# Optimization experiments

Measured on AMD Instinct MI355X. Metric: run time of the kernel, lower is better.

The kernel has to match this reference:

```python
import jax, jax.numpy as jnp
import numpy as np

N_NODES = 50000
N_EDGES = 500000
NFEAT = 128
NHID = 128
NOUT = 16


def setup_inputs() -> dict:
    key = jax.random.key(0)
    ks = jax.random.split(key, 8)
    x = jax.random.normal(ks[0], (N_NODES, NFEAT), dtype=jnp.float32)
    edge_src = jax.random.randint(ks[1], (N_EDGES,), 0, N_NODES, dtype=jnp.int32)
    edge_dst = jax.random.randint(ks[2], (N_EDGES,), 0, N_NODES, dtype=jnp.int32)
    edge_weight = jax.random.uniform(ks[3], (N_EDGES,), dtype=jnp.float32)
    # Glorot-ish init for linear weights, zero bias (PyG GCNConv default bias=0)
    def glorot(k, fan_in, fan_out):
        s = jnp.sqrt(6.0 / (fan_in + fan_out))
        return jax.random.uniform(k, (fan_in, fan_out), jnp.float32, -s, s)
    W1 = glorot(ks[4], NFEAT, NHID)
    W2 = glorot(ks[5], NHID, NHID)
    W3 = glorot(ks[6], NHID, NOUT)
    b1 = jnp.zeros((NHID,), jnp.float32)
    b2 = jnp.zeros((NHID,), jnp.float32)
    b3 = jnp.zeros((NOUT,), jnp.float32)
    return {"x": x, "edge_src": edge_src, "edge_dst": edge_dst,
            "edge_weight": edge_weight, "W1": W1, "b1": b1,
            "W2": W2, "b2": b2, "W3": W3, "b3": b3}


def gcn_conv(x, src, dst, ew, W, b):
    """PyG GCNConv: symmetric-normalized aggregation with self-loops (weight 1).

    out_i = sum_{(j->i)} d_i^{-1/2} w_ji d_j^{-1/2} (x_j W) + d_i^{-1} (x_i W) + b
    where d_i = 1 + sum of incoming edge weights.
    """
    n = x.shape[0]
    xw = x @ W                                            # [N, F_out]
    deg = jax.ops.segment_sum(ew, dst, num_segments=n) + 1.0  # self-loop weight 1
    dinv = jnp.where(deg > 0, jax.lax.rsqrt(deg), 0.0)    # d^{-1/2}
    norm = dinv[src] * ew * dinv[dst]                     # [E]
    agg = jax.ops.segment_sum(xw[src] * norm[:, None], dst, num_segments=n)
    self_loop = xw * (dinv * dinv)[:, None]               # d_i^{-1} * x_i W
    return agg + self_loop + b


def reference(x, edge_src, edge_dst, edge_weight, W1, b1, W2, b2, W3, b3):
    # Dropout layers are identity in eval mode.
    h = gcn_conv(x, edge_src, edge_dst, edge_weight, W1, b1)
    h = jax.nn.relu(h)
    h = gcn_conv(h, edge_src, edge_dst, edge_weight, W2, b2)
    h = jax.nn.relu(h)
    h = gcn_conv(h, edge_src, edge_dst, edge_weight, W3, b3)
    return jax.nn.log_softmax(h, axis=1)
```

## Files before the change

kernel.cpp:

```cpp
#include <hip/hip_runtime.h>
#include <math.h>

#define NN 50000
#define NE 500000
#define NF 128
#define NO 16
#define SCAN_B 1024
#define NPART 16

typedef _Float16 f16x8 __attribute__((ext_vector_type(8)));
typedef float f32x4 __attribute__((ext_vector_type(4)));


__global__ void k_count_rank(const int* __restrict__ dst, int* __restrict__ pcnt,
                             int* __restrict__ rank, int E) {
    int part = blockIdx.x & (NPART - 1);
    int e = blockIdx.x * blockDim.x + threadIdx.x;
    if (e < E) {
        int d = dst[e];
        rank[e] = atomicAdd(&pcnt[part * NN + d], 1);
    }
}

__global__ void k_combine(int* __restrict__ pcnt, int* __restrict__ counts, int N) {
    int n = blockIdx.x * blockDim.x + threadIdx.x;
    if (n < N) {
        int run = 0;
#pragma unroll
        for (int p = 0; p < NPART; ++p) {
            int v = pcnt[p * NN + n];
            pcnt[p * NN + n] = run;
            run += v;
        }
        counts[n] = run;
    }
}

__global__ void k_scan1(const int* __restrict__ counts, int* __restrict__ offs,
                        int* __restrict__ bsums, int N) {
    __shared__ int s[SCAN_B];
    int t = threadIdx.x;
    int i = blockIdx.x * SCAN_B + t;
    int c = (i < N) ? counts[i] : 0;
    s[t] = c;
    __syncthreads();
    for (int off = 1; off < SCAN_B; off <<= 1) {
        int x = (t >= off) ? s[t - off] : 0;
        __syncthreads();
        s[t] += x;
        __syncthreads();
    }
    if (i < N) offs[i] = s[t] - c;
    if (t == SCAN_B - 1) bsums[blockIdx.x] = s[t];
}

__global__ void k_scan2(int* __restrict__ bsums, int NB) {
    int t = threadIdx.x;
    int v = (t < NB) ? bsums[t] : 0;
    int orig = v;
#pragma unroll
    for (int off = 1; off < 64; off <<= 1) {
        int u = __shfl_up(v, off, 64);
        if (t >= off) v += u;
    }
    if (t < NB) bsums[t] = v - orig;
}

__global__ void k_scan3(int* __restrict__ offs, const int* __restrict__ bsums,
                        int N, int E) {
    int i = blockIdx.x * blockDim.x + threadIdx.x;
    if (i < N) {
        offs[i] = offs[i] + bsums[i >> 10];
    } else if (i == N) {
        offs[N] = E;
    }
}

__global__ void k_scatter(const int* __restrict__ src, const int* __restrict__ dst,
                          const float* __restrict__ ew, const int* __restrict__ offs,
                          const int* __restrict__ pcnt, const int* __restrict__ rank,
                          int* __restrict__ src_s, float* __restrict__ ew_s, int E) {
    int part = blockIdx.x & (NPART - 1);
    int e = blockIdx.x * blockDim.x + threadIdx.x;
    if (e < E) {
        int d = dst[e];
        int p = offs[d] + pcnt[part * NN + d] + rank[e];
        src_s[p] = src[e];
        ew_s[p]  = ew[e];
    }
}

__global__ void k_dinv_csr(const float* __restrict__ ew_s, const int* __restrict__ offs,
                           float* __restrict__ dinv, int N) {
    int n = blockIdx.x * blockDim.x + threadIdx.x;
    if (n < N) {
        float deg = 1.0f;
        int s = offs[n], e = offs[n + 1];
        for (int j = s; j < e; ++j) deg += ew_s[j];
        dinv[n] = rsqrtf(deg);
    }
}

__global__ void k_prep_w(const float* __restrict__ W1, const float* __restrict__ W2,
                         _Float16* __restrict__ W1T, _Float16* __restrict__ W2T) {
    int idx = blockIdx.x * 256 + threadIdx.x;
    int r = idx >> 7, c = idx & 127;
    W1T[(size_t)c * NF + r] = (_Float16)W1[idx];
    W2T[(size_t)c * NF + r] = (_Float16)W2[idx];
}


__device__ inline f16x8 afrag_load(const float* X, int row, int k0) {
    const float4* p = (const float4*)(X + (size_t)row * NF + k0);
    float4 a = p[0], b = p[1];
    f16x8 r;
    r[0] = (_Float16)a.x; r[1] = (_Float16)a.y; r[2] = (_Float16)a.z; r[3] = (_Float16)a.w;
    r[4] = (_Float16)b.x; r[5] = (_Float16)b.y; r[6] = (_Float16)b.z; r[7] = (_Float16)b.w;
    return r;
}
__device__ inline f16x8 afrag_load(const _Float16* X, int row, int k0) {
    return *(const f16x8*)(X + (size_t)row * NF + k0);
}

template <typename TA>
__global__ __launch_bounds__(256) void k_gemm_mfma(const TA* __restrict__ X,
                                                   const _Float16* __restrict__ WT,
                                                   const float* __restrict__ dinv,
                                                   _Float16* __restrict__ Z, int M) {
    __shared__ _Float16 ls[4][16 * NF];
    const int tid  = threadIdx.x;
    const int w    = tid >> 6;
    const int lane = tid & 63;
    const int n16  = lane & 15;
    const int quad = lane >> 4;
    const int r0   = blockIdx.x * 64 + w * 16;

    int arow = r0 + n16; if (arow > M - 1) arow = M - 1;

    f32x4 acc[8];
#pragma unroll
    for (int c = 0; c < 8; ++c) acc[c] = (f32x4){0.f, 0.f, 0.f, 0.f};

#pragma unroll
    for (int kk = 0; kk < 4; ++kk) {
        int k0 = kk * 32 + quad * 8;
        f16x8 a = afrag_load(X, arow, k0);
#pragma unroll
        for (int c = 0; c < 8; ++c) {
            f16x8 b = *(const f16x8*)(WT + (size_t)(c * 16 + n16) * NF + k0);
            acc[c] = __builtin_amdgcn_mfma_f32_16x16x32_f16(a, b, acc[c], 0, 0, 0);
        }
    }

#pragma unroll
    for (int reg = 0; reg < 4; ++reg) {
        int lrow = quad * 4 + reg;
        int grow = r0 + lrow; if (grow > M - 1) grow = M - 1;
        float di = dinv[grow];
#pragma unroll
        for (int c = 0; c < 8; ++c)
            ls[w][lrow * NF + c * 16 + n16] = (_Float16)(acc[c][reg] * di);
    }
    __syncthreads();
#pragma unroll
    for (int i = 0; i < 4; ++i) {
        int off16 = i * 64 + lane;
        int row = off16 >> 4;
        int grow = r0 + row;
        if (grow < M) {
            f16x8 v = *(const f16x8*)(&ls[w][off16 * 8]);
            *(f16x8*)(Z + (size_t)grow * NF + (off16 & 15) * 8) = v;
        }
    }
}

__global__ __launch_bounds__(256) void k_agg128h(const _Float16* __restrict__ z,
                                                 const float* __restrict__ dinv,
                                                 const int* __restrict__ offs,
                                                 const int* __restrict__ src_s,
                                                 const float* __restrict__ ew_s,
                                                 const float* __restrict__ bias,
                                                 _Float16* __restrict__ hout, int relu) {
    const int tid = threadIdx.x;
    const int ln = tid & 63;
    int n = __builtin_amdgcn_readfirstlane(blockIdx.x * 4 + (tid >> 6));

    union CV { unsigned int u; _Float16 h[2]; };

    float di = dinv[n];
    CV sv; sv.u = *(const unsigned int*)(z + (size_t)n * NF + ln * 2);
    float acc0 = (float)sv.h[0];
    float acc1 = (float)sv.h[1];

    int s = offs[n], e = offs[n + 1];
    int j = s;
    for (; j + 3 < e; j += 4) {
        int s0 = src_s[j], s1 = src_s[j + 1], s2 = src_s[j + 2], s3 = src_s[j + 3];
        float w0 = ew_s[j], w1 = ew_s[j + 1], w2 = ew_s[j + 2], w3 = ew_s[j + 3];
        CV u0, u1, u2, u3;
        u0.u = *(const unsigned int*)(z + (size_t)s0 * NF + ln * 2);
        u1.u = *(const unsigned int*)(z + (size_t)s1 * NF + ln * 2);
        u2.u = *(const unsigned int*)(z + (size_t)s2 * NF + ln * 2);
        u3.u = *(const unsigned int*)(z + (size_t)s3 * NF + ln * 2);
        acc0 = fmaf((float)u0.h[0], w0, acc0); acc1 = fmaf((float)u0.h[1], w0, acc1);
        acc0 = fmaf((float)u1.h[0], w1, acc0); acc1 = fmaf((float)u1.h[1], w1, acc1);
        acc0 = fmaf((float)u2.h[0], w2, acc0); acc1 = fmaf((float)u2.h[1], w2, acc1);
        acc0 = fmaf((float)u3.h[0], w3, acc0); acc1 = fmaf((float)u3.h[1], w3, acc1);
    }
    for (; j < e; ++j) {
        int s0 = src_s[j];
        float w0 = ew_s[j];
        CV u0; u0.u = *(const unsigned int*)(z + (size_t)s0 * NF + ln * 2);
        acc0 = fmaf((float)u0.h[0], w0, acc0);
        acc1 = fmaf((float)u0.h[1], w0, acc1);
    }
    float2 bb = *(const float2*)(bias + ln * 2);
    acc0 = fmaf(di, acc0, bb.x);
    acc1 = fmaf(di, acc1, bb.y);
    if (relu) { acc0 = fmaxf(acc0, 0.0f); acc1 = fmaxf(acc1, 0.0f); }
    CV o; o.h[0] = (_Float16)acc0; o.h[1] = (_Float16)acc1;
    *(unsigned int*)(hout + (size_t)n * NF + ln * 2) = o.u;
}

__global__ __launch_bounds__(256) void k_gemm16(const _Float16* __restrict__ H,
                                                const float* __restrict__ W3,
                                                const float* __restrict__ dinv,
                                                float* __restrict__ Z3, int M) {
    __shared__ float Wl[NF * NO];
    __shared__ float Hs[16 * 132];
    int tid = threadIdx.x;
    for (int i = tid; i < NF * NO; i += 256) Wl[i] = W3[i];
    int n0 = blockIdx.x * 16;
    {
        int row = tid >> 4, h8 = tid & 15;
        int gr = n0 + row; if (gr > M - 1) gr = M - 1;
        f16x8 v = *(const f16x8*)(H + (size_t)gr * NF + h8 * 8);
        float4 f0 = {(float)v[0], (float)v[1], (float)v[2], (float)v[3]};
        float4 f1 = {(float)v[4], (float)v[5], (float)v[6], (float)v[7]};
        *(float4*)(&Hs[row * 132 + h8 * 8])     = f0;
        *(float4*)(&Hs[row * 132 + h8 * 8 + 4]) = f1;
    }
    __syncthreads();
    int ln = tid >> 4, c = tid & 15;
    float acc = 0.0f;
#pragma unroll 8
    for (int k = 0; k < NF; ++k) acc = fmaf(Hs[ln * 132 + k], Wl[k * NO + c], acc);
    int n = n0 + ln;
    if (n < M) Z3[(size_t)n * NO + c] = acc * dinv[n];
}

__global__ __launch_bounds__(256) void k_agg16_ls(const float* __restrict__ z3,
                                                  const float* __restrict__ dinv,
                                                  const int* __restrict__ offs,
                                                  const int* __restrict__ src_s,
                                                  const float* __restrict__ ew_s,
                                                  const float* __restrict__ bias,
                                                  float* __restrict__ out) {
    int tid = threadIdx.x;
    int ln = tid >> 4, c = tid & 15;
    int n = blockIdx.x * 16 + ln;
    float acc = z3[(size_t)n * NO + c];
    int s = offs[n], e = offs[n + 1];
    for (int j = s; j < e; ++j) {
        acc = fmaf(z3[(size_t)src_s[j] * NO + c], ew_s[j], acc);
    }
    acc = fmaf(dinv[n], acc, bias[c]);
    float m = acc;
#pragma unroll
    for (int off = 8; off > 0; off >>= 1) m = fmaxf(m, __shfl_xor(m, off, 16));
    float ex = expf(acc - m);
    float ss = ex;
#pragma unroll
    for (int off = 8; off > 0; off >>= 1) ss += __shfl_xor(ss, off, 16);
    out[(size_t)n * NO + c] = acc - m - logf(ss);
}


extern "C" void kernel_launch(void* const* d_in, const int* in_sizes, int n_in,
                              void* d_out, int out_size, void* d_ws, size_t ws_size,
                              hipStream_t stream) {
    const float* x   = (const float*)d_in[0];
    const int*   esrc= (const int*)  d_in[1];
    const int*   edst= (const int*)  d_in[2];
    const float* ew  = (const float*)d_in[3];
    const float* W1  = (const float*)d_in[4];
    const float* b1  = (const float*)d_in[5];
    const float* W2  = (const float*)d_in[6];
    const float* b2  = (const float*)d_in[7];
    const float* W3  = (const float*)d_in[8];
    const float* b3  = (const float*)d_in[9];
    float* out = (float*)d_out;

    char* p = (char*)d_ws;
    _Float16* z   = (_Float16*)p; p += (size_t)NN * NF * 2;
    _Float16* h   = (_Float16*)p; p += (size_t)NN * NF * 2;
    float* z3     = (float*)p; p += (size_t)NN * NO * 4;
    float* dinv   = (float*)p; p += (size_t)NN * 4;
    float* ew_s   = (float*)p; p += (size_t)NE * 4;
    int*   src_s  = (int*)p;   p += (size_t)NE * 4;
    int*   rank   = (int*)p;   p += (size_t)NE * 4;
    int*   pcnt   = (int*)p;   p += (size_t)NPART * NN * 4;
    int*   counts = (int*)p;   p += (size_t)NN * 4;
    int*   offs   = (int*)p;   p += (size_t)(NN + 1) * 4;
    int*   bsums  = (int*)p;   p += 256;
    _Float16* W1T = (_Float16*)p; p += (size_t)NF * NF * 2;
    _Float16* W2T = (_Float16*)p; p += (size_t)NF * NF * 2;

    const int NB  = (NN + SCAN_B - 1) / SCAN_B;
    const int EBL = (NE + 255) / 256;
    const int NBL = (NN + 255) / 256;

    hipMemsetAsync(pcnt, 0, (size_t)NPART * NN * 4, stream);

    k_count_rank<<<EBL, 256, 0, stream>>>(edst, pcnt, rank, NE);
    k_combine<<<NBL, 256, 0, stream>>>(pcnt, counts, NN);
    k_scan1<<<NB, SCAN_B, 0, stream>>>(counts, offs, bsums, NN);
    k_scan2<<<1, 64, 0, stream>>>(bsums, NB);
    k_scan3<<<(NN + 256) / 256, 256, 0, stream>>>(offs, bsums, NN, NE);
    k_scatter<<<EBL, 256, 0, stream>>>(esrc, edst, ew, offs, pcnt, rank, src_s, ew_s, NE);
    k_dinv_csr<<<NBL, 256, 0, stream>>>(ew_s, offs, dinv, NN);
    k_prep_w<<<64, 256, 0, stream>>>(W1, W2, W1T, W2T);

    k_gemm_mfma<float><<<(NN + 63) / 64, 256, 0, stream>>>(x, W1T, dinv, z, NN);
    k_agg128h<<<NN / 4, 256, 0, stream>>>(z, dinv, offs, src_s, ew_s, b1, h, 1);
    k_gemm_mfma<_Float16><<<(NN + 63) / 64, 256, 0, stream>>>(h, W2T, dinv, z, NN);
    k_agg128h<<<NN / 4, 256, 0, stream>>>(z, dinv, offs, src_s, ew_s, b2, h, 1);
    k_gemm16<<<(NN + 15) / 16, 256, 0, stream>>>(h, W3, dinv, z3, NN);
    k_agg16_ls<<<NN / 16, 256, 0, stream>>>(z3, dinv, offs, src_s, ew_s, b3, out);
}
```

Baseline: 266.7 us.

## Fuse CSR build kernels, pack edge records, and store layer-3 features in fp16

Folds the weight transpose into the count kernel, merges the partition combine into the first scan, and bakes the prefix offsets into the per-partition counters so the scatter needs fewer lookups. Source index and weight are packed into one int2 record per edge. The 128-wide aggregation loads 64 records cooperatively per wave and broadcasts them with shuffles instead of loading each one per lane. The 16-wide layer-3 features are stored as fp16, halving gather traffic at some precision cost. Together these cut launch count and memory traffic in the preprocessing and aggregation stages.

```diff
diff --git a/kernel.cpp b/kernel.cpp
--- a/kernel.cpp
+++ b/kernel.cpp
@@ -7,106 +7,110 @@
 #define NO 16
 #define SCAN_B 1024
 #define NPART 16
+#define EBL 1954
 
 typedef _Float16 f16x8 __attribute__((ext_vector_type(8)));
 typedef float f32x4 __attribute__((ext_vector_type(4)));
 
 
 __global__ void k_count_rank(const int* __restrict__ dst, int* __restrict__ pcnt,
-                             int* __restrict__ rank, int E) {
+                             int* __restrict__ rank, int E,
+                             const float* __restrict__ W1, const float* __restrict__ W2,
+                             _Float16* __restrict__ W1T, _Float16* __restrict__ W2T) {
+    int b = blockIdx.x;
+    if (b < EBL) {
+        int part = b & (NPART - 1);
+        int e = b * 256 + threadIdx.x;
+        if (e < E) {
+            int d = dst[e];
+            rank[e] = atomicAdd(&pcnt[part * NN + d], 1);
+        }
+    } else {
+        int idx = (b - EBL) * 256 + threadIdx.x;
+        int r = idx >> 7, c = idx & 127;
+        W1T[(size_t)c * NF + r] = (_Float16)W1[idx];
+        W2T[(size_t)c * NF + r] = (_Float16)W2[idx];
+    }
+}
+
+__global__ void k_scan1f(int* __restrict__ pcnt, int* __restrict__ offs_p,
+                         int* __restrict__ bsums, int N) {
+    __shared__ int sm[SCAN_B];
+    int t = threadIdx.x;
+    int i = blockIdx.x * SCAN_B + t;
+    int c = 0;
+    if (i < N) {
+        int run = 0;
+#pragma unroll
+        for (int p = 0; p < NPART; ++p) {
+            int v = pcnt[p * NN + i];
+            pcnt[p * NN + i] = run;
+            run += v;
+        }
+        c = run;
+    }
+    sm[t] = c;
+    __syncthreads();
+    for (int off = 1; off < SCAN_B; off <<= 1) {
+        int x = (t >= off) ? sm[t - off] : 0;
+        __syncthreads();
+        sm[t] += x;
+        __syncthreads();
+    }
+    if (i < N) offs_p[i] = sm[t] - c;
+    if (t == SCAN_B - 1) bsums[blockIdx.x] = sm[t];
+}
+
+__global__ void k_scan2(int* __restrict__ bsums, int NB) {
+    int t = threadIdx.x;
+    int v = (t < NB) ? bsums[t] : 0;
+    int orig = v;
+#pragma unroll
+    for (int off = 1; off < 64; off <<= 1) {
+        int u = __shfl_up(v, off, 64);
+        if (t >= off) v += u;
+    }
+    if (t < NB) bsums[t] = v - orig;
+}
+
+__global__ void k_scan3x(const int* __restrict__ offs_p, const int* __restrict__ bsums,
+                         int* __restrict__ pcnt, int* __restrict__ offs_f, int E) {
+    int i = blockIdx.x * blockDim.x + threadIdx.x;
+    if (i < NPART * NN) {
+        int p = i / NN;
+        int n = i - p * NN;
+        int v = offs_p[n] + bsums[n >> 10];
+        pcnt[i] += v;
+        if (p == 0) offs_f[n] = v;
+    } else if (i == NPART * NN) {
+        offs_f[NN] = E;
+    }
+}
+
+__global__ void k_scatter(const int* __restrict__ src, const int* __restrict__ dst,
+                          const float* __restrict__ ew, const int* __restrict__ pcnt,
+                          const int* __restrict__ rank, int2* __restrict__ edge_rec, int E) {
     int part = blockIdx.x & (NPART - 1);
     int e = blockIdx.x * blockDim.x + threadIdx.x;
     if (e < E) {
         int d = dst[e];
-        rank[e] = atomicAdd(&pcnt[part * NN + d], 1);
-    }
-}
-
-__global__ void k_combine(int* __restrict__ pcnt, int* __restrict__ counts, int N) {
-    int n = blockIdx.x * blockDim.x + threadIdx.x;
-    if (n < N) {
-        int run = 0;
-#pragma unroll
-        for (int p = 0; p < NPART; ++p) {
-            int v = pcnt[p * NN + n];
-            pcnt[p * NN + n] = run;
-            run += v;
-        }
-        counts[n] = run;
-    }
-}
-
-__global__ void k_scan1(const int* __restrict__ counts, int* __restrict__ offs,
-                        int* __restrict__ bsums, int N) {
-    __shared__ int s[SCAN_B];
-    int t = threadIdx.x;
-    int i = blockIdx.x * SCAN_B + t;
-    int c = (i < N) ? counts[i] : 0;
-    s[t] = c;
-    __syncthreads();
-    for (int off = 1; off < SCAN_B; off <<= 1) {
-        int x = (t >= off) ? s[t - off] : 0;
-        __syncthreads();
-        s[t] += x;
-        __syncthreads();
-    }
-    if (i < N) offs[i] = s[t] - c;
-    if (t == SCAN_B - 1) bsums[blockIdx.x] = s[t];
-}
-
-__global__ void k_scan2(int* __restrict__ bsums, int NB) {
-    int t = threadIdx.x;
-    int v = (t < NB) ? bsums[t] : 0;
-    int orig = v;
-#pragma unroll
-    for (int off = 1; off < 64; off <<= 1) {
-        int u = __shfl_up(v, off, 64);
-        if (t >= off) v += u;
-    }
-    if (t < NB) bsums[t] = v - orig;
-}
-
-__global__ void k_scan3(int* __restrict__ offs, const int* __restrict__ bsums,
-                        int N, int E) {
-    int i = blockIdx.x * blockDim.x + threadIdx.x;
-    if (i < N) {
-        offs[i] = offs[i] + bsums[i >> 10];
-    } else if (i == N) {
-        offs[N] = E;
-    }
-}
-
-__global__ void k_scatter(const int* __restrict__ src, const int* __restrict__ dst,
-                          const float* __restrict__ ew, const int* __restrict__ offs,
-                          const int* __restrict__ pcnt, const int* __restrict__ rank,
-                          int* __restrict__ src_s, float* __restrict__ ew_s, int E) {
-    int part = blockIdx.x & (NPART - 1);
-    int e = blockIdx.x * blockDim.x + threadIdx.x;
-    if (e < E) {
-        int d = dst[e];
-        int p = offs[d] + pcnt[part * NN + d] + rank[e];
-        src_s[p] = src[e];
-        ew_s[p]  = ew[e];
-    }
-}
-
-__global__ void k_dinv_csr(const float* __restrict__ ew_s, const int* __restrict__ offs,
+        int pos = pcnt[part * NN + d] + rank[e];
+        int2 r;
+        r.x = src[e];
+        r.y = __float_as_int(ew[e]);
+        edge_rec[pos] = r;
+    }
+}
+
+__global__ void k_dinv_csr(const int2* __restrict__ edge_rec, const int* __restrict__ offs,
                            float* __restrict__ dinv, int N) {
     int n = blockIdx.x * blockDim.x + threadIdx.x;
     if (n < N) {
         float deg = 1.0f;
         int s = offs[n], e = offs[n + 1];
-        for (int j = s; j < e; ++j) deg += ew_s[j];
+        for (int j = s; j < e; ++j) deg += __int_as_float(edge_rec[j].y);
         dinv[n] = rsqrtf(deg);
     }
-}
-
-__global__ void k_prep_w(const float* __restrict__ W1, const float* __restrict__ W2,
-                         _Float16* __restrict__ W1T, _Float16* __restrict__ W2T) {
-    int idx = blockIdx.x * 256 + threadIdx.x;
-    int r = idx >> 7, c = idx & 127;
-    W1T[(size_t)c * NF + r] = (_Float16)W1[idx];
-    W2T[(size_t)c * NF + r] = (_Float16)W2[idx];
 }
 
 
@@ -177,8 +181,7 @@
 __global__ __launch_bounds__(256) void k_agg128h(const _Float16* __restrict__ z,
                                                  const float* __restrict__ dinv,
                                                  const int* __restrict__ offs,
-                                                 const int* __restrict__ src_s,
-                                                 const float* __restrict__ ew_s,
+                                                 const int2* __restrict__ edge_rec,
                                                  const float* __restrict__ bias,
                                                  _Float16* __restrict__ hout, int relu) {
     const int tid = threadIdx.x;
@@ -188,44 +191,53 @@
     union CV { unsigned int u; _Float16 h[2]; };
 
     float di = dinv[n];
-    CV sv; sv.u = *(const unsigned int*)(z + (size_t)n * NF + ln * 2);
+    CV sv; sv.u = *(const unsigned int*)(z + ((size_t)n << 7) + ln * 2);
     float acc0 = (float)sv.h[0];
     float acc1 = (float)sv.h[1];
 
     int s = offs[n], e = offs[n + 1];
-    int j = s;
-    for (; j + 3 < e; j += 4) {
-        int s0 = src_s[j], s1 = src_s[j + 1], s2 = src_s[j + 2], s3 = src_s[j + 3];
-        float w0 = ew_s[j], w1 = ew_s[j + 1], w2 = ew_s[j + 2], w3 = ew_s[j + 3];
-        CV u0, u1, u2, u3;
-        u0.u = *(const unsigned int*)(z + (size_t)s0 * NF + ln * 2);
-        u1.u = *(const unsigned int*)(z + (size_t)s1 * NF + ln * 2);
-        u2.u = *(const unsigned int*)(z + (size_t)s2 * NF + ln * 2);
-        u3.u = *(const unsigned int*)(z + (size_t)s3 * NF + ln * 2);
-        acc0 = fmaf((float)u0.h[0], w0, acc0); acc1 = fmaf((float)u0.h[1], w0, acc1);
-        acc0 = fmaf((float)u1.h[0], w1, acc0); acc1 = fmaf((float)u1.h[1], w1, acc1);
-        acc0 = fmaf((float)u2.h[0], w2, acc0); acc1 = fmaf((float)u2.h[1], w2, acc1);
-        acc0 = fmaf((float)u3.h[0], w3, acc0); acc1 = fmaf((float)u3.h[1], w3, acc1);
-    }
-    for (; j < e; ++j) {
-        int s0 = src_s[j];
-        float w0 = ew_s[j];
-        CV u0; u0.u = *(const unsigned int*)(z + (size_t)s0 * NF + ln * 2);
-        acc0 = fmaf((float)u0.h[0], w0, acc0);
-        acc1 = fmaf((float)u0.h[1], w0, acc1);
+    for (int base = s; base < e; base += 64) {
+        int cnt = e - base; if (cnt > 64) cnt = 64;
+        int2 rec = {0, 0};
+        if (ln < cnt) rec = edge_rec[base + ln];
+        int   my_s = rec.x;
+        float my_w = __int_as_float(rec.y);
+        int k = 0;
+        for (; k + 3 < cnt; k += 4) {
+            int s0 = __shfl(my_s, k, 64),     s1 = __shfl(my_s, k + 1, 64);
+            int s2 = __shfl(my_s, k + 2, 64), s3 = __shfl(my_s, k + 3, 64);
+            float w0 = __shfl(my_w, k, 64),     w1 = __shfl(my_w, k + 1, 64);
+            float w2 = __shfl(my_w, k + 2, 64), w3 = __shfl(my_w, k + 3, 64);
+            CV u0, u1, u2, u3;
+            u0.u = *(const unsigned int*)(z + ((size_t)s0 << 7) + ln * 2);
+            u1.u = *(const unsigned int*)(z + ((size_t)s1 << 7) + ln * 2);
+            u2.u = *(const unsigned int*)(z + ((size_t)s2 << 7) + ln * 2);
+            u3.u = *(const unsigned int*)(z + ((size_t)s3 << 7) + ln * 2);
+            acc0 = fmaf((float)u0.h[0], w0, acc0); acc1 = fmaf((float)u0.h[1], w0, acc1);
+            acc0 = fmaf((float)u1.h[0], w1, acc0); acc1 = fmaf((float)u1.h[1], w1, acc1);
+            acc0 = fmaf((float)u2.h[0], w2, acc0); acc1 = fmaf((float)u2.h[1], w2, acc1);
+            acc0 = fmaf((float)u3.h[0], w3, acc0); acc1 = fmaf((float)u3.h[1], w3, acc1);
+        }
+        for (; k < cnt; ++k) {
+            int   s0 = __shfl(my_s, k, 64);
+            float w0 = __shfl(my_w, k, 64);
+            CV u0; u0.u = *(const unsigned int*)(z + ((size_t)s0 << 7) + ln * 2);
+            acc0 = fmaf((float)u0.h[0], w0, acc0);
+            acc1 = fmaf((float)u0.h[1], w0, acc1);
+        }
     }
     float2 bb = *(const float2*)(bias + ln * 2);
     acc0 = fmaf(di, acc0, bb.x);
     acc1 = fmaf(di, acc1, bb.y);
     if (relu) { acc0 = fmaxf(acc0, 0.0f); acc1 = fmaxf(acc1, 0.0f); }
     CV o; o.h[0] = (_Float16)acc0; o.h[1] = (_Float16)acc1;
-    *(unsigned int*)(hout + (size_t)n * NF + ln * 2) = o.u;
+    *(unsigned int*)(hout + ((size_t)n << 7) + ln * 2) = o.u;
 }
 
 __global__ __launch_bounds__(256) void k_gemm16(const _Float16* __restrict__ H,
                                                 const float* __restrict__ W3,
                                                 const float* __restrict__ dinv,
-                                                float* __restrict__ Z3, int M) {
+                                                _Float16* __restrict__ Z3, int M) {
     __shared__ float Wl[NF * NO];
     __shared__ float Hs[16 * 132];
     int tid = threadIdx.x;
@@ -246,23 +258,29 @@
 #pragma unroll 8
     for (int k = 0; k < NF; ++k) acc = fmaf(Hs[ln * 132 + k], Wl[k * NO + c], acc);
     int n = n0 + ln;
-    if (n < M) Z3[(size_t)n * NO + c] = acc * dinv[n];
-}
-
-__global__ __launch_bounds__(256) void k_agg16_ls(const float* __restrict__ z3,
+    if (n < M) Z3[(size_t)n * NO + c] = (_Float16)(acc * dinv[n]);
+}
+
+__global__ __launch_bounds__(256) void k_agg16_ls(const _Float16* __restrict__ z3,
                                                   const float* __restrict__ dinv,
                                                   const int* __restrict__ offs,
-                                                  const int* __restrict__ src_s,
-                                                  const float* __restrict__ ew_s,
+                                                  const int2* __restrict__ edge_rec,
                                                   const float* __restrict__ bias,
                                                   float* __restrict__ out) {
     int tid = threadIdx.x;
     int ln = tid >> 4, c = tid & 15;
     int n = blockIdx.x * 16 + ln;
-    float acc = z3[(size_t)n * NO + c];
+    float acc = (float)z3[(size_t)n * NO + c];
     int s = offs[n], e = offs[n + 1];
-    for (int j = s; j < e; ++j) {
-        acc = fmaf(z3[(size_t)src_s[j] * NO + c], ew_s[j], acc);
+    int j = s;
+    for (; j + 1 < e; j += 2) {
+        int2 r0 = edge_rec[j], r1 = edge_rec[j + 1];
+        acc = fmaf((float)z3[((size_t)r0.x << 4) + c], __int_as_float(r0.y), acc);
+        acc = fmaf((float)z3[((size_t)r1.x << 4) + c], __int_as_float(r1.y), acc);
+    }
+    if (j < e) {
+        int2 r0 = edge_rec[j];
+        acc = fmaf((float)z3[((size_t)r0.x << 4) + c], __int_as_float(r0.y), acc);
     }
     acc = fmaf(dinv[n], acc, bias[c]);
     float m = acc;
@@ -294,37 +312,33 @@
     char* p = (char*)d_ws;
     _Float16* z   = (_Float16*)p; p += (size_t)NN * NF * 2;
     _Float16* h   = (_Float16*)p; p += (size_t)NN * NF * 2;
-    float* z3     = (float*)p; p += (size_t)NN * NO * 4;
+    _Float16* z3  = (_Float16*)p; p += (size_t)NN * NO * 2;
     float* dinv   = (float*)p; p += (size_t)NN * 4;
-    float* ew_s   = (float*)p; p += (size_t)NE * 4;
-    int*   src_s  = (int*)p;   p += (size_t)NE * 4;
+    int2*  edge_rec = (int2*)p; p += (size_t)NE * 8;
     int*   rank   = (int*)p;   p += (size_t)NE * 4;
     int*   pcnt   = (int*)p;   p += (size_t)NPART * NN * 4;
-    int*   counts = (int*)p;   p += (size_t)NN * 4;
-    int*   offs   = (int*)p;   p += (size_t)(NN + 1) * 4;
+    int*   offs_p = (int*)p;   p += (size_t)(NN + 1) * 4;
+    int*   offs_f = (int*)p;   p += (size_t)(NN + 1) * 4;
     int*   bsums  = (int*)p;   p += 256;
     _Float16* W1T = (_Float16*)p; p += (size_t)NF * NF * 2;
     _Float16* W2T = (_Float16*)p; p += (size_t)NF * NF * 2;
 
     const int NB  = (NN + SCAN_B - 1) / SCAN_B;
-    const int EBL = (NE + 255) / 256;
     const int NBL = (NN + 255) / 256;
 
     hipMemsetAsync(pcnt, 0, (size_t)NPART * NN * 4, stream);
 
-    k_count_rank<<<EBL, 256, 0, stream>>>(edst, pcnt, rank, NE);
-    k_combine<<<NBL, 256, 0, stream>>>(pcnt, counts, NN);
-    k_scan1<<<NB, SCAN_B, 0, stream>>>(counts, offs, bsums, NN);
+    k_count_rank<<<EBL + 64, 256, 0, stream>>>(edst, pcnt, rank, NE, W1, W2, W1T, W2T);
+    k_scan1f<<<NB, SCAN_B, 0, stream>>>(pcnt, offs_p, bsums, NN);
     k_scan2<<<1, 64, 0, stream>>>(bsums, NB);
-    k_scan3<<<(NN + 256) / 256, 256, 0, stream>>>(offs, bsums, NN, NE);
-    k_scatter<<<EBL, 256, 0, stream>>>(esrc, edst, ew, offs, pcnt, rank, src_s, ew_s, NE);
-    k_dinv_csr<<<NBL, 256, 0, stream>>>(ew_s, offs, dinv, NN);
-    k_prep_w<<<64, 256, 0, stream>>>(W1, W2, W1T, W2T);
+    k_scan3x<<<(NPART * NN + 256) / 256, 256, 0, stream>>>(offs_p, bsums, pcnt, offs_f, NE);
+    k_scatter<<<EBL, 256, 0, stream>>>(esrc, edst, ew, pcnt, rank, edge_rec, NE);
+    k_dinv_csr<<<NBL, 256, 0, stream>>>(edge_rec, offs_f, dinv, NN);
 
     k_gemm_mfma<float><<<(NN + 63) / 64, 256, 0, stream>>>(x, W1T, dinv, z, NN);
-    k_agg128h<<<NN / 4, 256, 0, stream>>>(z, dinv, offs, src_s, ew_s, b1, h, 1);
+    k_agg128h<<<NN / 4, 256, 0, stream>>>(z, dinv, offs_f, edge_rec, b1, h, 1);
     k_gemm_mfma<_Float16><<<(NN + 63) / 64, 256, 0, stream>>>(h, W2T, dinv, z, NN);
-    k_agg128h<<<NN / 4, 256, 0, stream>>>(z, dinv, offs, src_s, ew_s, b2, h, 1);
+    k_agg128h<<<NN / 4, 256, 0, stream>>>(z, dinv, offs_f, edge_rec, b2, h, 1);
     k_gemm16<<<(NN + 15) / 16, 256, 0, stream>>>(h, W3, dinv, z3, NN);
-    k_agg16_ls<<<NN / 16, 256, 0, stream>>>(z3, dinv, offs, src_s, ew_s, b3, out);
-}
+    k_agg16_ls<<<NN / 16, 256, 0, stream>>>(z3, dinv, offs_f, edge_rec, b3, out);
+}
```

Result: faster. 252.3 us (-5.4%).
